# Kernel optimization log

Measured on AMD Instinct MI355X. Metric: run time of the kernel, lower is better.

## Reference

```python
import jax, jax.numpy as jnp
import numpy as np

N_Q = 9      # qubits -> state dim 512
N_L = 10     # circuit layers
DIM = 2 ** N_Q
B = 16384    # batch
N_CLS = 10


def _apply_1q(psi, U, q):
    # psi: [B, 2,...,2] (N_Q qubit axes); U: [2,2] complex
    psi = jnp.moveaxis(psi, q + 1, 1)
    shp = psi.shape
    psi = jnp.einsum('ij,bjk->bik', U, psi.reshape(shp[0], 2, -1)).reshape(shp)
    return jnp.moveaxis(psi, 1, q + 1)


def _apply_2q(psi, U, q0, q1):
    # U: [4,4] complex acting on (q0, q1)
    psi = jnp.moveaxis(psi, (q0 + 1, q1 + 1), (1, 2))
    shp = psi.shape
    psi = jnp.einsum('ij,bjk->bik', U, psi.reshape(shp[0], 4, -1)).reshape(shp)
    return jnp.moveaxis(psi, (1, 2), (q0 + 1, q1 + 1))


def _rot_mat(phi, theta, omega):
    # PennyLane Rot = RZ(omega) RY(theta) RZ(phi)
    c, s = jnp.cos(theta / 2), jnp.sin(theta / 2)
    a, b = (phi + omega) / 2, (phi - omega) / 2
    return jnp.stack([
        jnp.stack([jnp.exp(-1j * a) * c, -jnp.exp(1j * b) * s]),
        jnp.stack([jnp.exp(-1j * b) * s, jnp.exp(1j * a) * c]),
    ]).astype(jnp.complex64)


def _crx_mat(t):
    c, s = jnp.cos(t / 2), jnp.sin(t / 2)
    rx = jnp.stack([jnp.stack([c + 0j, -1j * s]),
                    jnp.stack([-1j * s, c + 0j])]).astype(jnp.complex64)
    return jnp.eye(4, dtype=jnp.complex64).at[2:, 2:].set(rx)


def _layer(psi, rot_n, crx_n):
    for i in range(N_Q):
        psi = _apply_1q(psi, _rot_mat(rot_n[i, 0], rot_n[i, 1], rot_n[i, 2]), i)
    for i in range(N_Q):
        psi = _apply_2q(psi, _crx_mat(crx_n[i, 0]), i, (i + 1) % N_Q)
    return psi


def _circuit(x, rot, crx):
    # AmplitudeEmbedding(normalize=True)
    psi = (x / jnp.linalg.norm(x, axis=1, keepdims=True)).astype(jnp.complex64)
    psi = psi.reshape((x.shape[0],) + (2,) * N_Q)
    for n in range(N_L):
        psi = _layer(psi, rot[n], crx[n])
    probs = psi.real ** 2 + psi.imag ** 2
    # <Z_q> = P(bit_q = 0) - P(bit_q = 1)
    zs = []
    for q in range(N_Q):
        axes = tuple(a for a in range(1, N_Q + 1) if a != q + 1)
        p = probs.sum(axis=axes)  # [B, 2]
        zs.append(p[:, 0] - p[:, 1])
    return jnp.stack(zs, axis=1)  # [B, N_Q]


def setup_inputs() -> dict:
    key = jax.random.key(0)
    k0, k1, k2, k3, k4 = jax.random.split(key, 5)
    x = jax.random.normal(k0, (B, DIM), jnp.float32)
    rot = jax.random.normal(k1, (N_L, N_Q, 3), jnp.float32)
    crx = jax.random.normal(k2, (N_L, N_Q, 1), jnp.float32)
    fc_w = jax.random.normal(k3, (N_CLS, N_Q), jnp.float32) * 0.3
    fc_b = jax.random.normal(k4, (N_CLS,), jnp.float32) * 0.1
    return {"x": x, "rot": rot, "crx": crx, "fc_w": fc_w, "fc_b": fc_b}


def reference(x, rot, crx, fc_w, fc_b):
    z = _circuit(x, rot, crx)          # [B, 9]
    logits = z @ fc_w.T + fc_b         # [B, 10]
    return jax.nn.log_softmax(logits, axis=1)
```

## Files before the change

### kernel.cpp

```cpp
#include <hip/hip_runtime.h>
#include <hip/hip_bf16.h>
#include <math.h>

#define NQ 9
#define NL 10
#define DIM 512
#define NCLS 10
#define B_TOT 16384

#define A_OFF   ((size_t)0)
#define BT_OFF  ((size_t)16 << 20)
#define ZP_OFF  ((size_t)32 << 20)
#define WS_NEED (((size_t)96) << 20)

__device__ __forceinline__ float shx(float v, int m) { return __shfl_xor(v, m, 64); }

__device__ __forceinline__ int looks_bf16(const void* p, int count) {
  const unsigned short* u = (const unsigned short*)p;
  int n = count < 64 ? count : 64;
  int good = 0;
  for (int i = 0; i < n; ++i) {
    unsigned short v = u[i];
    int e = (v >> 7) & 0xFF;
    good += (e >= 100 && e <= 140) || ((v & 0x7FFF) == 0);
  }
  return good * 8 >= n * 7;
}

__device__ __forceinline__ float ld(const void* p, int i, int isbf) {
  if (isbf) return __uint_as_float(((unsigned)((const unsigned short*)p)[i]) << 16);
  return ((const float*)p)[i];
}

template<int M>
__device__ __forceinline__ void rot_x(float (&sr)[8], float (&si)[8], const float* u) {
  float4 uA = *(const float4*)u;
  float4 uB = *(const float4*)(u + 4);
  bool hi = (threadIdx.x & M) != 0;
  float ar = hi ? uB.z : uA.x, ai = hi ? uB.w : uA.y;
  float br = hi ? uB.x : uA.z, bi = hi ? uB.y : uA.w;
#pragma unroll
  for (int r = 0; r < 8; ++r) {
    float pr = shx(sr[r], M), pi = shx(si[r], M);
    float nr = ar * sr[r] - ai * si[r] + br * pr - bi * pi;
    float ni = ar * si[r] + ai * sr[r] + br * pi + bi * pr;
    sr[r] = nr; si[r] = ni;
  }
}
template<int S>
__device__ __forceinline__ void rot_r(float (&sr)[8], float (&si)[8], const float* u) {
  float4 uA = *(const float4*)u;
  float4 uB = *(const float4*)(u + 4);
#pragma unroll
  for (int r0 = 0; r0 < 8; ++r0) {
    if (r0 & S) continue;
    int r1 = r0 + S;
    float a0r = sr[r0], a0i = si[r0], a1r = sr[r1], a1i = si[r1];
    sr[r0] = uA.x * a0r - uA.y * a0i + uA.z * a1r - uA.w * a1i;
    si[r0] = uA.x * a0i + uA.y * a0r + uA.z * a1i + uA.w * a1r;
    sr[r1] = uB.x * a0r - uB.y * a0i + uB.z * a1r - uB.w * a1i;
    si[r1] = uB.x * a0i + uB.y * a0r + uB.z * a1i + uB.w * a1r;
  }
}
template<int MC, int MT>
__device__ __forceinline__ void crx_ll(float (&sr)[8], float (&si)[8], const float* cs) {
  bool ctrl = (threadIdx.x & MC) != 0;
  float c = ctrl ? cs[0] : 1.0f;
  float s = ctrl ? cs[1] : 0.0f;
#pragma unroll
  for (int r = 0; r < 8; ++r) {
    float pr = shx(sr[r], MT), pi = shx(si[r], MT);
    float nr = c * sr[r] + s * pi;
    float ni = c * si[r] - s * pr;
    sr[r] = nr; si[r] = ni;
  }
}
template<int MC, int ST>
__device__ __forceinline__ void crx_lr(float (&sr)[8], float (&si)[8], const float* cs) {
  bool ctrl = (threadIdx.x & MC) != 0;
  float c = ctrl ? cs[0] : 1.0f;
  float s = ctrl ? cs[1] : 0.0f;
#pragma unroll
  for (int r0 = 0; r0 < 8; ++r0) {
    if (r0 & ST) continue;
    int r1 = r0 + ST;
    float a0r = sr[r0], a0i = si[r0], a1r = sr[r1], a1i = si[r1];
    sr[r0] = c * a0r + s * a1i;  si[r0] = c * a0i - s * a1r;
    sr[r1] = c * a1r + s * a0i;  si[r1] = c * a1i - s * a0r;
  }
}
template<int PC, int ST>
__device__ __forceinline__ void crx_rr(float (&sr)[8], float (&si)[8], const float* cs) {
  float c = cs[0], s = cs[1];
#pragma unroll
  for (int r0 = 0; r0 < 8; ++r0) {
    if (r0 & ST) continue;
    if (!((r0 >> PC) & 1)) continue;
    int r1 = r0 + ST;
    float a0r = sr[r0], a0i = si[r0], a1r = sr[r1], a1i = si[r1];
    sr[r0] = c * a0r + s * a1i;  si[r0] = c * a0i - s * a1r;
    sr[r1] = c * a1r + s * a0i;  si[r1] = c * a1i - s * a0r;
  }
}
template<int PC, int MT>
__device__ __forceinline__ void crx_rl(float (&sr)[8], float (&si)[8], const float* cs) {
  float c = cs[0], s = cs[1];
#pragma unroll
  for (int r = 0; r < 8; ++r) {
    if (!((r >> PC) & 1)) continue;
    float pr = shx(sr[r], MT), pi = shx(si[r], MT);
    float nr = c * sr[r] + s * pi;
    float ni = c * si[r] - s * pr;
    sr[r] = nr; si[r] = ni;
  }
}

__device__ __forceinline__ void build_gates(const void* rot, const void* crx,
                                            float* gU, float* gCS) {
  int tid = threadIdx.x;
  __shared__ int gflags[2];
  if (tid == 0) {
    gflags[0] = looks_bf16(rot, NL * NQ * 3);
    gflags[1] = looks_bf16(crx, NL * NQ);
  }
  __syncthreads();
  if (tid < NL * NQ) {
    int frot = gflags[0], fcrx = gflags[1];
    float phi = ld(rot, tid * 3 + 0, frot);
    float th  = ld(rot, tid * 3 + 1, frot);
    float om  = ld(rot, tid * 3 + 2, frot);
    float c = cosf(0.5f * th), s = sinf(0.5f * th);
    float a = 0.5f * (phi + om), b = 0.5f * (phi - om);
    float ca = cosf(a), sa = sinf(a), cb = cosf(b), sb = sinf(b);
    float* u = gU + tid * 8;
    u[0] =  ca * c; u[1] = -sa * c;
    u[2] = -cb * s; u[3] = -sb * s;
    u[4] =  cb * s; u[5] = -sb * s;
    u[6] =  ca * c; u[7] =  sa * c;
    float t2 = 0.5f * ld(crx, tid, fcrx);
    gCS[tid * 2 + 0] = cosf(t2);
    gCS[tid * 2 + 1] = sinf(t2);
  }
  __syncthreads();
}

__device__ __forceinline__ void run_circuit(float (&sr)[8], float (&si)[8],
                                            const float* gU, const float* gCS) {
#pragma unroll 1
  for (int n = 0; n < NL; ++n) {
    const float* U  = gU  + n * NQ * 8;
    const float* CS = gCS + n * NQ * 2;
    rot_x<32>(sr, si, U + 0 * 8);
    rot_x<16>(sr, si, U + 1 * 8);
    rot_x< 8>(sr, si, U + 2 * 8);
    rot_x< 4>(sr, si, U + 3 * 8);
    rot_x< 2>(sr, si, U + 4 * 8);
    rot_x< 1>(sr, si, U + 5 * 8);
    rot_r< 4>(sr, si, U + 6 * 8);
    rot_r< 2>(sr, si, U + 7 * 8);
    rot_r< 1>(sr, si, U + 8 * 8);
    crx_ll<32, 16>(sr, si, CS + 0 * 2);
    crx_ll<16,  8>(sr, si, CS + 1 * 2);
    crx_ll< 8,  4>(sr, si, CS + 2 * 2);
    crx_ll< 4,  2>(sr, si, CS + 3 * 2);
    crx_ll< 2,  1>(sr, si, CS + 4 * 2);
    crx_lr< 1,  4>(sr, si, CS + 5 * 2);
    crx_rr< 2,  2>(sr, si, CS + 6 * 2);
    crx_rr< 1,  1>(sr, si, CS + 7 * 2);
    crx_rl< 0, 32>(sr, si, CS + 8 * 2);
  }
}

template<int M>
__device__ __forceinline__ void rot_lane2(float (&sr)[2], float (&si)[2], const float* u) {
  float4 uA = *(const float4*)u;
  float4 uB = *(const float4*)(u + 4);
  bool hi = (threadIdx.x & M) != 0;
  float ar = hi ? uB.z : uA.x, ai = hi ? uB.w : uA.y;
  float br = hi ? uB.x : uA.z, bi = hi ? uB.y : uA.w;
#pragma unroll
  for (int r = 0; r < 2; ++r) {
    float pr = shx(sr[r], M), pi = shx(si[r], M);
    float nr = ar * sr[r] - ai * si[r] + br * pr - bi * pi;
    float ni = ar * si[r] + ai * sr[r] + br * pi + bi * pr;
    sr[r] = nr; si[r] = ni;
  }
}
__device__ __forceinline__ void rot_reg2(float (&sr)[2], float (&si)[2], const float* u) {
  float4 uA = *(const float4*)u;
  float4 uB = *(const float4*)(u + 4);
  float a0r = sr[0], a0i = si[0], a1r = sr[1], a1i = si[1];
  sr[0] = uA.x * a0r - uA.y * a0i + uA.z * a1r - uA.w * a1i;
  si[0] = uA.x * a0i + uA.y * a0r + uA.z * a1i + uA.w * a1r;
  sr[1] = uB.x * a0r - uB.y * a0i + uB.z * a1r - uB.w * a1i;
  si[1] = uB.x * a0i + uB.y * a0r + uB.z * a1i + uB.w * a1r;
}
__device__ __forceinline__ void crx_lane2(float (&sr)[2], float (&si)[2],
                                          float c, float s, int MT) {
#pragma unroll
  for (int r = 0; r < 2; ++r) {
    float pr = shx(sr[r], MT), pi = shx(si[r], MT);
    float nr = c * sr[r] + s * pi;
    float ni = c * si[r] - s * pr;
    sr[r] = nr; si[r] = ni;
  }
}
__device__ __forceinline__ void crx_reg2(float (&sr)[2], float (&si)[2], float c, float s) {
  float a0r = sr[0], a0i = si[0], a1r = sr[1], a1i = si[1];
  sr[0] = c * a0r + s * a1i;  si[0] = c * a0i - s * a1r;
  sr[1] = c * a1r + s * a0i;  si[1] = c * a1i - s * a0r;
}

__global__ __launch_bounds__(256) void prep_kernel(const void* __restrict__ x,
                                                   const void* __restrict__ rot,
                                                   const void* __restrict__ crx,
                                                   __hip_bfloat16* __restrict__ A,
                                                   __hip_bfloat16* __restrict__ BT) {
  int tid = threadIdx.x;
  if (blockIdx.x < DIM) {
    __shared__ __align__(16) float gU[NL * NQ * 8];
    __shared__ __align__(16) float gCS[NL * NQ * 2];
    __shared__ float sRe[DIM], sIm[DIM];
    build_gates(rot, crx, gU, gCS);
    int lane = tid & 63, wv = tid >> 6;
    int idx0 = wv * 128 + lane * 2;
    int k = blockIdx.x;
    float sr[2], si[2];
    sr[0] = (idx0 == k) ? 1.f : 0.f;
    sr[1] = (idx0 + 1 == k) ? 1.f : 0.f;
    si[0] = si[1] = 0.f;
#pragma unroll 1
    for (int n = 0; n < NL; ++n) {
      const float* U  = gU  + n * NQ * 8;
      const float* CS = gCS + n * NQ * 2;
      __syncthreads();
      sRe[idx0] = sr[0]; sIm[idx0] = si[0];
      sRe[idx0 + 1] = sr[1]; sIm[idx0 + 1] = si[1];
      __syncthreads();
      {
        const float* U0 = U; const float* U1 = U + 8;
        int a = wv >> 1, b = wv & 1;
        float mr[4], mi[4];
#pragma unroll
        for (int w2 = 0; w2 < 4; ++w2) {
          int a2 = w2 >> 1, b2 = w2 & 1;
          float u0r = U0[(a * 2 + a2) * 2], u0i = U0[(a * 2 + a2) * 2 + 1];
          float u1r = U1[(b * 2 + b2) * 2], u1i = U1[(b * 2 + b2) * 2 + 1];
          mr[w2] = u0r * u1r - u0i * u1i;
          mi[w2] = u0r * u1i + u0i * u1r;
        }
#pragma unroll
        for (int r = 0; r < 2; ++r) {
          float nr = 0.f, ni = 0.f;
#pragma unroll
          for (int w2 = 0; w2 < 4; ++w2) {
            float xr = sRe[w2 * 128 + lane * 2 + r];
            float xi = sIm[w2 * 128 + lane * 2 + r];
            nr += mr[w2] * xr - mi[w2] * xi;
            ni += mr[w2] * xi + mi[w2] * xr;
          }
          sr[r] = nr; si[r] = ni;
        }
      }
      rot_lane2<32>(sr, si, U + 2 * 8);
      rot_lane2<16>(sr, si, U + 3 * 8);
      rot_lane2< 8>(sr, si, U + 4 * 8);
      rot_lane2< 4>(sr, si, U + 5 * 8);
      rot_lane2< 2>(sr, si, U + 6 * 8);
      rot_lane2< 1>(sr, si, U + 7 * 8);
      rot_reg2(sr, si, U + 8 * 8);
      __syncthreads();
      sRe[idx0] = sr[0]; sIm[idx0] = si[0];
      sRe[idx0 + 1] = sr[1]; sIm[idx0 + 1] = si[1];
      __syncthreads();
      {
        float c = (wv & 2) ? CS[0] : 1.f, s = (wv & 2) ? CS[1] : 0.f;
        int p0 = (wv ^ 1) * 128 + lane * 2;
#pragma unroll
        for (int r = 0; r < 2; ++r) {
          float pr = sRe[p0 + r], pi = sIm[p0 + r];
          float nr = c * sr[r] + s * pi;
          float ni = c * si[r] - s * pr;
          sr[r] = nr; si[r] = ni;
        }
      }
      { float c = (wv & 1) ? CS[2] : 1.f, s = (wv & 1) ? CS[3] : 0.f;
        crx_lane2(sr, si, c, s, 32); }
      { bool ct = (lane & 32); crx_lane2(sr, si, ct ? CS[4] : 1.f, ct ? CS[5] : 0.f, 16); }
      { bool ct = (lane & 16); crx_lane2(sr, si, ct ? CS[6] : 1.f, ct ? CS[7] : 0.f, 8); }
      { bool ct = (lane &  8); crx_lane2(sr, si, ct ? CS[8] : 1.f, ct ? CS[9] : 0.f, 4); }
      { bool ct = (lane &  4); crx_lane2(sr, si, ct ? CS[10] : 1.f, ct ? CS[11] : 0.f, 2); }
      { bool ct = (lane &  2); crx_lane2(sr, si, ct ? CS[12] : 1.f, ct ? CS[13] : 0.f, 1); }
      { bool ct = (lane & 1); crx_reg2(sr, si, ct ? CS[14] : 1.f, ct ? CS[15] : 0.f); }
      __syncthreads();
      sRe[idx0] = sr[0]; sIm[idx0] = si[0];
      sRe[idx0 + 1] = sr[1]; sIm[idx0 + 1] = si[1];
      __syncthreads();
      {
        float c = CS[16], s = CS[17];
        int p1 = (wv ^ 2) * 128 + lane * 2 + 1;
        float pr = sRe[p1], pi = sIm[p1];
        float nr = c * sr[1] + s * pi;
        float ni = c * si[1] - s * pr;
        sr[1] = nr; si[1] = ni;
      }
    }
#pragma unroll
    for (int r = 0; r < 2; ++r) {
      int j = idx0 + r;
      BT[(size_t)j * DIM + k]         = __float2bfloat16(sr[r]);
      BT[(size_t)(DIM + j) * DIM + k] = __float2bfloat16(si[r]);
    }
  } else {
    __shared__ int fx;
    if (tid == 0) fx = looks_bf16(x, B_TOT * DIM);
    __syncthreads();
    size_t i0 = ((size_t)(blockIdx.x - DIM) * 256 + tid) * 8;
    if (fx) {
      *(uint4*)(A + i0) = *(const uint4*)((const unsigned short*)x + i0);
    } else {
      const float4* src = (const float4*)((const float*)x + i0);
      float4 a = src[0], b = src[1];
      __hip_bfloat16 o[8];
      o[0] = __float2bfloat16(a.x); o[1] = __float2bfloat16(a.y);
      o[2] = __float2bfloat16(a.z); o[3] = __float2bfloat16(a.w);
      o[4] = __float2bfloat16(b.x); o[5] = __float2bfloat16(b.y);
      o[6] = __float2bfloat16(b.z); o[7] = __float2bfloat16(b.w);
      *(uint4*)(A + i0) = *(uint4*)o;
    }
  }
}

using frag8 = __attribute__((ext_vector_type(8))) short;
using frag4 = __attribute__((ext_vector_type(4))) float;

typedef __attribute__((address_space(1))) const unsigned int GU32;
typedef __attribute__((address_space(3))) unsigned int LU32;
__device__ __forceinline__ void async16(const void* g, void* l) {
  __builtin_amdgcn_global_load_lds((GU32*)g, (LU32*)l, 16, 0, 0);
}

#define PPITCH 136
#define PANEL (128 * 32)

__global__ __launch_bounds__(256) void gemm_z_kernel(const unsigned short* __restrict__ A,
                                                     const unsigned short* __restrict__ BT,
                                                     float* __restrict__ Zp) {
  __shared__ __align__(16) unsigned short lsm[128 * PPITCH + 16 * PPITCH];
  unsigned short* lA0 = lsm;
  unsigned short* lA1 = lsm + PANEL;
  unsigned short* lB0 = lsm + 2 * PANEL;
  unsigned short* lB1 = lsm + 3 * PANEL;
  unsigned short* pA  = lsm;
  unsigned short* STm = lsm + 128 * PPITCH;
  int bid = blockIdx.x;
  int xcd = bid & 7;
  int slot = bid >> 3;
  int n0 = (slot & 7) * 128;
  int m0 = (xcd * 16 + (slot >> 3)) * 128;
  int tid = threadIdx.x;
  int wv = tid >> 6, lane = tid & 63;
  int wm = wv >> 1, wn = wv & 1;
  int row = lane & 15, quad = lane >> 4;
  for (int i = tid; i < 16 * 128; i += 256) {
    int q = i >> 7, k2 = i & 127;
    int j = (n0 + k2) & 511;
    float sg = (q < 9) ? (((j >> (8 - q)) & 1) ? -1.f : 1.f) : (q == 9 ? 1.f : 0.f);
    __hip_bfloat16 h = __float2bfloat16(sg);
    STm[q * PPITCH + k2] = *(unsigned short*)&h;
  }
  int srow = wv * 32 + (lane >> 2);
  int scol = (lane & 3) * 8;
  const unsigned short* gA = A + (size_t)(m0 + srow) * 512 + scol;
  const unsigned short* gB = BT + (size_t)(n0 + srow) * 512 + scol;
  frag4 acc[4][4] = {};
#pragma unroll 1
  for (int k0 = 0; k0 < 512; k0 += 64) {
    __syncthreads();
    async16(gA + k0,                 &lA0[(wv * 32) * 32]);
    async16(gA + k0 + 16 * 512,      &lA0[(wv * 32 + 16) * 32]);
    async16(gA + k0 + 32,            &lA1[(wv * 32) * 32]);
    async16(gA + k0 + 32 + 16 * 512, &lA1[(wv * 32 + 16) * 32]);
    async16(gB + k0,                 &lB0[(wv * 32) * 32]);
    async16(gB + k0 + 16 * 512,      &lB0[(wv * 32 + 16) * 32]);
    async16(gB + k0 + 32,            &lB1[(wv * 32) * 32]);
    async16(gB + k0 + 32 + 16 * 512, &lB1[(wv * 32 + 16) * 32]);
    __syncthreads();
    {
      frag8 af[4], bf[4];
#pragma unroll
      for (int i = 0; i < 4; ++i) {
        af[i] = *(const frag8*)(&lA0[(wm * 64 + i * 16 + row) * 32 + quad * 8]);
        bf[i] = *(const frag8*)(&lB0[(wn * 64 + i * 16 + row) * 32 + quad * 8]);
      }
#pragma unroll
      for (int mi = 0; mi < 4; ++mi)
#pragma unroll
        for (int ni = 0; ni < 4; ++ni)
          acc[mi][ni] = __builtin_amdgcn_mfma_f32_16x16x32_bf16(af[mi], bf[ni],
                                                                acc[mi][ni], 0, 0, 0);
    }
    {
      frag8 af[4], bf[4];
#pragma unroll
      for (int i = 0; i < 4; ++i) {
        af[i] = *(const frag8*)(&lA1[(wm * 64 + i * 16 + row) * 32 + quad * 8]);
        bf[i] = *(const frag8*)(&lB1[(wn * 64 + i * 16 + row) * 32 + quad * 8]);
      }
#pragma unroll
      for (int mi = 0; mi < 4; ++mi)
#pragma unroll
        for (int ni = 0; ni < 4; ++ni)
          acc[mi][ni] = __builtin_amdgcn_mfma_f32_16x16x32_bf16(af[mi], bf[ni],
                                                                acc[mi][ni], 0, 0, 0);
    }
  }
  __syncthreads();
#pragma unroll
  for (int mi = 0; mi < 4; ++mi)
#pragma unroll
    for (int ni = 0; ni < 4; ++ni)
#pragma unroll
      for (int rg = 0; rg < 4; ++rg) {
        float v = acc[mi][ni][rg];
        float p = v * v;
        int mrow = wm * 64 + mi * 16 + quad * 4 + rg;
        int k2 = wn * 64 + ni * 16 + row;
        __hip_bfloat16 h = __float2bfloat16(p);
        pA[mrow * PPITCH + k2] = *(unsigned short*)&h;
      }
  __syncthreads();
  frag8 b2[4];
#pragma unroll
  for (int kk = 0; kk < 4; ++kk)
    b2[kk] = *(const frag8*)(&STm[row * PPITCH + kk * 32 + quad * 8]);
  frag4 zacc2[2] = {};
#pragma unroll
  for (int t = 0; t < 2; ++t) {
    int mt = wv + t * 4;
#pragma unroll
    for (int kk = 0; kk < 4; ++kk) {
      frag8 a2 = *(const frag8*)(&pA[(mt * 16 + row) * PPITCH + kk * 32 + quad * 8]);
      zacc2[t] = __builtin_amdgcn_mfma_f32_16x16x32_bf16(a2, b2[kk], zacc2[t], 0, 0, 0);
    }
  }
  int panel = n0 >> 7;
  if (row < 10) {
#pragma unroll
    for (int t = 0; t < 2; ++t) {
      int mt = wv + t * 4;
#pragma unroll
      for (int rg = 0; rg < 4; ++rg) {
        int mrow = m0 + mt * 16 + quad * 4 + rg;
        Zp[(size_t)panel * (B_TOT * 10) + (size_t)mrow * 10 + row] = zacc2[t][rg];
      }
    }
  }
}

__global__ __launch_bounds__(256) void zred_kernel(const float* __restrict__ Zp,
                                                   const void* __restrict__ fcw,
                                                   const void* __restrict__ fcb,
                                                   float* __restrict__ out) {
  __shared__ int flags[2];
  __shared__ float sW[NCLS * NQ];
  __shared__ float sB[NCLS];
  int tid = threadIdx.x;
  if (tid == 0) {
    flags[0] = looks_bf16(fcw, NCLS * NQ);
    flags[1] = looks_bf16(fcb, NCLS);
  }
  __syncthreads();
  if (tid < NCLS * NQ) sW[tid] = ld(fcw, tid, flags[0]);
  if (tid < NCLS)      sB[tid] = ld(fcb, tid, flags[1]);
  __syncthreads();
  int row = blockIdx.x * 256 + tid;
  float z[10];
#pragma unroll
  for (int q = 0; q < 10; ++q) z[q] = 0.f;
#pragma unroll
  for (int pnl = 0; pnl < 8; ++pnl) {
    const float* p = Zp + (size_t)pnl * (B_TOT * 10) + (size_t)row * 10;
#pragma unroll
    for (int q = 0; q < 10; ++q) z[q] += p[q];
  }
  float invP = 1.0f / z[9];
#pragma unroll
  for (int q = 0; q < NQ; ++q) z[q] *= invP;
  float lg[NCLS], mx = -1e30f;
#pragma unroll
  for (int k = 0; k < NCLS; ++k) {
    float t = sB[k];
#pragma unroll
    for (int q = 0; q < NQ; ++q) t += z[q] * sW[k * NQ + q];
    lg[k] = t; mx = fmaxf(mx, t);
  }
  float se = 0.f;
#pragma unroll
  for (int k = 0; k < NCLS; ++k) se += expf(lg[k] - mx);
  float lse = mx + logf(se);
#pragma unroll
  for (int k = 0; k < NCLS; ++k) out[(size_t)row * NCLS + k] = lg[k] - lse;
}

__global__ __launch_bounds__(256) void qnn_kernel(
    const void* __restrict__ x, const void* __restrict__ rot,
    const void* __restrict__ crx, const void* __restrict__ fcw,
    const void* __restrict__ fcb, float* __restrict__ out) {
  __shared__ __align__(16) float gU[NL * NQ * 8];
  __shared__ __align__(16) float gCS[NL * NQ * 2];
  __shared__ int flags[3];
  int tid = threadIdx.x;
  if (tid == 0) {
    flags[0] = looks_bf16(x, B_TOT * DIM);
    flags[1] = looks_bf16(fcw, NCLS * NQ);
    flags[2] = looks_bf16(fcb, NCLS);
  }
  build_gates(rot, crx, gU, gCS);
  __syncthreads();
  int wid = (blockIdx.x * blockDim.x + tid) >> 6;
  int lane = tid & 63;
  float sr[8], si[8];
  if (flags[0]) {
    const uint4 u = *(const uint4*)((const unsigned short*)x + (size_t)wid * DIM + lane * 8);
    sr[0] = __uint_as_float(u.x << 16); sr[1] = __uint_as_float(u.x & 0xffff0000u);
    sr[2] = __uint_as_float(u.y << 16); sr[3] = __uint_as_float(u.y & 0xffff0000u);
    sr[4] = __uint_as_float(u.z << 16); sr[5] = __uint_as_float(u.z & 0xffff0000u);
    sr[6] = __uint_as_float(u.w << 16); sr[7] = __uint_as_float(u.w & 0xffff0000u);
  } else {
    const float4* xf = (const float4*)((const float*)x + (size_t)wid * DIM) + lane * 2;
    float4 a = xf[0], b = xf[1];
    sr[0] = a.x; sr[1] = a.y; sr[2] = a.z; sr[3] = a.w;
    sr[4] = b.x; sr[5] = b.y; sr[6] = b.z; sr[7] = b.w;
  }
  float nrm = 0.f;
#pragma unroll
  for (int r = 0; r < 8; ++r) { nrm += sr[r] * sr[r]; si[r] = 0.f; }
#pragma unroll
  for (int m = 1; m < 64; m <<= 1) nrm += shx(nrm, m);
  float inv = rsqrtf(nrm);
  inv = inv * (1.5f - 0.5f * nrm * inv * inv);
#pragma unroll
  for (int r = 0; r < 8; ++r) sr[r] *= inv;
  run_circuit(sr, si, gU, gCS);
  float p[8], P = 0.f;
#pragma unroll
  for (int r = 0; r < 8; ++r) { p[r] = sr[r] * sr[r] + si[r] * si[r]; P += p[r]; }
  float z[NQ];
#pragma unroll
  for (int q = 0; q < 6; ++q) z[q] = (lane & (32 >> q)) ? -P : P;
  z[6] = z[7] = z[8] = 0.f;
#pragma unroll
  for (int r = 0; r < 8; ++r) {
    z[6] += (r & 4) ? -p[r] : p[r];
    z[7] += (r & 2) ? -p[r] : p[r];
    z[8] += (r & 1) ? -p[r] : p[r];
  }
#pragma unroll
  for (int m = 1; m < 64; m <<= 1) {
#pragma unroll
    for (int q = 0; q < NQ; ++q) z[q] += shx(z[q], m);
  }
  int ffw = flags[1], ffb = flags[2];
  float lg[NCLS], mx = -1e30f;
#pragma unroll
  for (int k = 0; k < NCLS; ++k) {
    float t = ld(fcb, k, ffb);
#pragma unroll
    for (int q = 0; q < NQ; ++q) t += z[q] * ld(fcw, k * NQ + q, ffw);
    lg[k] = t; mx = fmaxf(mx, t);
  }
  float se = 0.f;
#pragma unroll
  for (int k = 0; k < NCLS; ++k) se += expf(lg[k] - mx);
  float lse = mx + logf(se);
  if (lane < NCLS) out[(size_t)wid * NCLS + lane] = lg[lane] - lse;
}

extern "C" void kernel_launch(void* const* d_in, const int* in_sizes, int n_in,
                              void* d_out, int out_size, void* d_ws, size_t ws_size,
                              hipStream_t stream) {
  const void* x   = d_in[0];
  const void* rot = d_in[1];
  const void* crx = d_in[2];
  const void* fcw = d_in[3];
  const void* fcb = d_in[4];
  float* out = (float*)d_out;
  if (ws_size >= WS_NEED) {
    __hip_bfloat16* A  = (__hip_bfloat16*)((char*)d_ws + A_OFF);
    __hip_bfloat16* BT = (__hip_bfloat16*)((char*)d_ws + BT_OFF);
    float*          Zp = (float*)((char*)d_ws + ZP_OFF);
    prep_kernel<<<DIM + (B_TOT * DIM) / (256 * 8), 256, 0, stream>>>(x, rot, crx, A, BT);
    gemm_z_kernel<<<(B_TOT / 128) * (1024 / 128), 256, 0, stream>>>(
        (const unsigned short*)A, (const unsigned short*)BT, Zp);
    zred_kernel<<<B_TOT / 256, 256, 0, stream>>>(Zp, fcw, fcb, out);
  } else {
    qnn_kernel<<<(B_TOT * 64) / 256, 256, 0, stream>>>(x, rot, crx, fcw, fcb, out);
  }
}
```

Before: 142.0 us.

## Use 512-thread blocks with fused 3-qubit gate matrices in unitary prep

The prep kernel now uses 512 threads, one amplitude per thread, instead of 256 threads holding two each. It precomputes 8x8 fused matrices for the first three Rot gates and for the first two CRX gates, and folds the last CRX of each layer into the next layer's load. This cuts the number of shared-memory round trips and barriers per layer. In exchange each thread does more multiply-adds per fused stage, the block uses more shared memory, and the conversion blocks are halved in count but doubled in size.

```diff
diff --git a/kernel.cpp b/kernel.cpp
--- a/kernel.cpp
+++ b/kernel.cpp
@@ -172,46 +172,25 @@
 }
 
 template<int M>
-__device__ __forceinline__ void rot_lane2(float (&sr)[2], float (&si)[2], const float* u) {
+__device__ __forceinline__ void rot1(float& sr, float& si, const float* u) {
   float4 uA = *(const float4*)u;
   float4 uB = *(const float4*)(u + 4);
   bool hi = (threadIdx.x & M) != 0;
   float ar = hi ? uB.z : uA.x, ai = hi ? uB.w : uA.y;
   float br = hi ? uB.x : uA.z, bi = hi ? uB.y : uA.w;
-#pragma unroll
-  for (int r = 0; r < 2; ++r) {
-    float pr = shx(sr[r], M), pi = shx(si[r], M);
-    float nr = ar * sr[r] - ai * si[r] + br * pr - bi * pi;
-    float ni = ar * si[r] + ai * sr[r] + br * pi + bi * pr;
-    sr[r] = nr; si[r] = ni;
-  }
-}
-__device__ __forceinline__ void rot_reg2(float (&sr)[2], float (&si)[2], const float* u) {
-  float4 uA = *(const float4*)u;
-  float4 uB = *(const float4*)(u + 4);
-  float a0r = sr[0], a0i = si[0], a1r = sr[1], a1i = si[1];
-  sr[0] = uA.x * a0r - uA.y * a0i + uA.z * a1r - uA.w * a1i;
-  si[0] = uA.x * a0i + uA.y * a0r + uA.z * a1i + uA.w * a1r;
-  sr[1] = uB.x * a0r - uB.y * a0i + uB.z * a1r - uB.w * a1i;
-  si[1] = uB.x * a0i + uB.y * a0r + uB.z * a1i + uB.w * a1r;
-}
-__device__ __forceinline__ void crx_lane2(float (&sr)[2], float (&si)[2],
-                                          float c, float s, int MT) {
-#pragma unroll
-  for (int r = 0; r < 2; ++r) {
-    float pr = shx(sr[r], MT), pi = shx(si[r], MT);
-    float nr = c * sr[r] + s * pi;
-    float ni = c * si[r] - s * pr;
-    sr[r] = nr; si[r] = ni;
-  }
-}
-__device__ __forceinline__ void crx_reg2(float (&sr)[2], float (&si)[2], float c, float s) {
-  float a0r = sr[0], a0i = si[0], a1r = sr[1], a1i = si[1];
-  sr[0] = c * a0r + s * a1i;  si[0] = c * a0i - s * a1r;
-  sr[1] = c * a1r + s * a0i;  si[1] = c * a1i - s * a0r;
-}
-
-__global__ __launch_bounds__(256) void prep_kernel(const void* __restrict__ x,
+  float pr = shx(sr, M), pi = shx(si, M);
+  float nr = ar * sr - ai * si + br * pr - bi * pi;
+  float ni = ar * si + ai * sr + br * pi + bi * pr;
+  sr = nr; si = ni;
+}
+__device__ __forceinline__ void crx1(float& sr, float& si, float c, float s, int MT) {
+  float pr = shx(sr, MT), pi = shx(si, MT);
+  float nr = c * sr + s * pi;
+  float ni = c * si - s * pr;
+  sr = nr; si = ni;
+}
+
+__global__ __launch_bounds__(512) void prep_kernel(const void* __restrict__ x,
                                                    const void* __restrict__ rot,
                                                    const void* __restrict__ crx,
                                                    __hip_bfloat16* __restrict__ A,
@@ -220,102 +199,118 @@
   if (blockIdx.x < DIM) {
     __shared__ __align__(16) float gU[NL * NQ * 8];
     __shared__ __align__(16) float gCS[NL * NQ * 2];
-    __shared__ float sRe[DIM], sIm[DIM];
+    __shared__ __align__(16) float gM8[NL * 64 * 2];
+    __shared__ __align__(16) float gM8c[NL * 64 * 2];
+    __shared__ float bRe[2][DIM], bIm[2][DIM];
     build_gates(rot, crx, gU, gCS);
+    for (int it = tid; it < NL * 64; it += 512) {
+      int n = it >> 6, e = it & 63;
+      int w = e >> 3, w2 = e & 7;
+      int a = (w >> 2) & 1, b = (w >> 1) & 1, c = w & 1;
+      int a2 = (w2 >> 2) & 1, b2 = (w2 >> 1) & 1, c2 = w2 & 1;
+      const float* U0 = gU + (n * 9 + 0) * 8;
+      const float* U1 = gU + (n * 9 + 1) * 8;
+      const float* U2 = gU + (n * 9 + 2) * 8;
+      float r0 = U0[(a * 2 + a2) * 2],  i0 = U0[(a * 2 + a2) * 2 + 1];
+      float r1 = U1[(b * 2 + b2) * 2],  i1 = U1[(b * 2 + b2) * 2 + 1];
+      float r2 = U2[(c * 2 + c2) * 2],  i2 = U2[(c * 2 + c2) * 2 + 1];
+      float rr = r0 * r1 - i0 * i1, ri = r0 * i1 + i0 * r1;
+      gM8[(n * 64 + e) * 2]     = rr * r2 - ri * i2;
+      gM8[(n * 64 + e) * 2 + 1] = rr * i2 + ri * r2;
+      const float* CSn = gCS + n * 18;
+      float c1 = CSn[0], s1 = CSn[1], c2v = CSn[2], s2v = CSn[3];
+      float f1r, f1i, f2r, f2i;
+      if (a == 0) { f1r = (b == b2) ? 1.f : 0.f; f1i = 0.f; }
+      else        { f1r = (b == b2) ? c1 : 0.f;  f1i = (b == b2) ? 0.f : -s1; }
+      if (b == 0) { f2r = (c == c2) ? 1.f : 0.f; f2i = 0.f; }
+      else        { f2r = (c == c2) ? c2v : 0.f; f2i = (c == c2) ? 0.f : -s2v; }
+      float Mr = (a == a2) ? (f1r * f2r - f1i * f2i) : 0.f;
+      float Mi = (a == a2) ? (f1r * f2i + f1i * f2r) : 0.f;
+      gM8c[(n * 64 + e) * 2]     = Mr;
+      gM8c[(n * 64 + e) * 2 + 1] = Mi;
+    }
+    __syncthreads();
     int lane = tid & 63, wv = tid >> 6;
-    int idx0 = wv * 128 + lane * 2;
     int k = blockIdx.x;
-    float sr[2], si[2];
-    sr[0] = (idx0 == k) ? 1.f : 0.f;
-    sr[1] = (idx0 + 1 == k) ? 1.f : 0.f;
-    si[0] = si[1] = 0.f;
+    float sr = (tid == k) ? 1.f : 0.f, si = 0.f;
 #pragma unroll 1
     for (int n = 0; n < NL; ++n) {
-      const float* U  = gU  + n * NQ * 8;
-      const float* CS = gCS + n * NQ * 2;
+      const float* CS  = gCS + n * 18;
+      const float* CSp = gCS + (n - 1) * 18;
+      bRe[0][tid] = sr; bIm[0][tid] = si;
       __syncthreads();
-      sRe[idx0] = sr[0]; sIm[idx0] = si[0];
-      sRe[idx0 + 1] = sr[1]; sIm[idx0 + 1] = si[1];
+      float xr[8], xi[8];
+#pragma unroll
+      for (int w2 = 0; w2 < 8; ++w2) {
+        xr[w2] = bRe[0][w2 * 64 + lane];
+        xi[w2] = bIm[0][w2 * 64 + lane];
+      }
+      if (n > 0 && (lane & 1)) {
+        float cp = CSp[16], sp = CSp[17];
+        float tr[8], ti[8];
+#pragma unroll
+        for (int w2 = 0; w2 < 8; ++w2) {
+          tr[w2] = cp * xr[w2] + sp * xi[w2 ^ 4];
+          ti[w2] = cp * xi[w2] - sp * xr[w2 ^ 4];
+        }
+#pragma unroll
+        for (int w2 = 0; w2 < 8; ++w2) { xr[w2] = tr[w2]; xi[w2] = ti[w2]; }
+      }
+      {
+        const float* M = gM8 + n * 128 + wv * 16;
+        float nr = 0.f, ni = 0.f;
+#pragma unroll
+        for (int w2 = 0; w2 < 8; ++w2) {
+          float mr = M[w2 * 2], mi2 = M[w2 * 2 + 1];
+          nr += mr * xr[w2] - mi2 * xi[w2];
+          ni += mr * xi[w2] + mi2 * xr[w2];
+        }
+        sr = nr; si = ni;
+      }
+      rot1<32>(sr, si, gU + (n * 9 + 3) * 8);
+      rot1<16>(sr, si, gU + (n * 9 + 4) * 8);
+      rot1< 8>(sr, si, gU + (n * 9 + 5) * 8);
+      rot1< 4>(sr, si, gU + (n * 9 + 6) * 8);
+      rot1< 2>(sr, si, gU + (n * 9 + 7) * 8);
+      rot1< 1>(sr, si, gU + (n * 9 + 8) * 8);
+      bRe[1][tid] = sr; bIm[1][tid] = si;
       __syncthreads();
       {
-        const float* U0 = U; const float* U1 = U + 8;
-        int a = wv >> 1, b = wv & 1;
-        float mr[4], mi[4];
-#pragma unroll
-        for (int w2 = 0; w2 < 4; ++w2) {
-          int a2 = w2 >> 1, b2 = w2 & 1;
-          float u0r = U0[(a * 2 + a2) * 2], u0i = U0[(a * 2 + a2) * 2 + 1];
-          float u1r = U1[(b * 2 + b2) * 2], u1i = U1[(b * 2 + b2) * 2 + 1];
-          mr[w2] = u0r * u1r - u0i * u1i;
-          mi[w2] = u0r * u1i + u0i * u1r;
+        const float* M = gM8c + n * 128 + wv * 16;
+        float nr = 0.f, ni = 0.f;
+#pragma unroll
+        for (int w2 = 0; w2 < 8; ++w2) {
+          float vr = bRe[1][w2 * 64 + lane], vi = bIm[1][w2 * 64 + lane];
+          float mr = M[w2 * 2], mi2 = M[w2 * 2 + 1];
+          nr += mr * vr - mi2 * vi;
+          ni += mr * vi + mi2 * vr;
         }
-#pragma unroll
-        for (int r = 0; r < 2; ++r) {
-          float nr = 0.f, ni = 0.f;
-#pragma unroll
-          for (int w2 = 0; w2 < 4; ++w2) {
-            float xr = sRe[w2 * 128 + lane * 2 + r];
-            float xi = sIm[w2 * 128 + lane * 2 + r];
-            nr += mr[w2] * xr - mi[w2] * xi;
-            ni += mr[w2] * xi + mi[w2] * xr;
-          }
-          sr[r] = nr; si[r] = ni;
-        }
-      }
-      rot_lane2<32>(sr, si, U + 2 * 8);
-      rot_lane2<16>(sr, si, U + 3 * 8);
-      rot_lane2< 8>(sr, si, U + 4 * 8);
-      rot_lane2< 4>(sr, si, U + 5 * 8);
-      rot_lane2< 2>(sr, si, U + 6 * 8);
-      rot_lane2< 1>(sr, si, U + 7 * 8);
-      rot_reg2(sr, si, U + 8 * 8);
-      __syncthreads();
-      sRe[idx0] = sr[0]; sIm[idx0] = si[0];
-      sRe[idx0 + 1] = sr[1]; sIm[idx0 + 1] = si[1];
-      __syncthreads();
-      {
-        float c = (wv & 2) ? CS[0] : 1.f, s = (wv & 2) ? CS[1] : 0.f;
-        int p0 = (wv ^ 1) * 128 + lane * 2;
-#pragma unroll
-        for (int r = 0; r < 2; ++r) {
-          float pr = sRe[p0 + r], pi = sIm[p0 + r];
-          float nr = c * sr[r] + s * pi;
-          float ni = c * si[r] - s * pr;
-          sr[r] = nr; si[r] = ni;
-        }
-      }
-      { float c = (wv & 1) ? CS[2] : 1.f, s = (wv & 1) ? CS[3] : 0.f;
-        crx_lane2(sr, si, c, s, 32); }
-      { bool ct = (lane & 32); crx_lane2(sr, si, ct ? CS[4] : 1.f, ct ? CS[5] : 0.f, 16); }
-      { bool ct = (lane & 16); crx_lane2(sr, si, ct ? CS[6] : 1.f, ct ? CS[7] : 0.f, 8); }
-      { bool ct = (lane &  8); crx_lane2(sr, si, ct ? CS[8] : 1.f, ct ? CS[9] : 0.f, 4); }
-      { bool ct = (lane &  4); crx_lane2(sr, si, ct ? CS[10] : 1.f, ct ? CS[11] : 0.f, 2); }
-      { bool ct = (lane &  2); crx_lane2(sr, si, ct ? CS[12] : 1.f, ct ? CS[13] : 0.f, 1); }
-      { bool ct = (lane & 1); crx_reg2(sr, si, ct ? CS[14] : 1.f, ct ? CS[15] : 0.f); }
-      __syncthreads();
-      sRe[idx0] = sr[0]; sIm[idx0] = si[0];
-      sRe[idx0 + 1] = sr[1]; sIm[idx0 + 1] = si[1];
-      __syncthreads();
-      {
-        float c = CS[16], s = CS[17];
-        int p1 = (wv ^ 2) * 128 + lane * 2 + 1;
-        float pr = sRe[p1], pi = sIm[p1];
-        float nr = c * sr[1] + s * pi;
-        float ni = c * si[1] - s * pr;
-        sr[1] = nr; si[1] = ni;
-      }
-    }
-#pragma unroll
-    for (int r = 0; r < 2; ++r) {
-      int j = idx0 + r;
-      BT[(size_t)j * DIM + k]         = __float2bfloat16(sr[r]);
-      BT[(size_t)(DIM + j) * DIM + k] = __float2bfloat16(si[r]);
-    }
+        sr = nr; si = ni;
+      }
+      { bool ct = wv & 1;    crx1(sr, si, ct ? CS[4] : 1.f,  ct ? CS[5] : 0.f, 32); }
+      { bool ct = lane & 32; crx1(sr, si, ct ? CS[6] : 1.f,  ct ? CS[7] : 0.f, 16); }
+      { bool ct = lane & 16; crx1(sr, si, ct ? CS[8] : 1.f,  ct ? CS[9] : 0.f,  8); }
+      { bool ct = lane &  8; crx1(sr, si, ct ? CS[10] : 1.f, ct ? CS[11] : 0.f, 4); }
+      { bool ct = lane &  4; crx1(sr, si, ct ? CS[12] : 1.f, ct ? CS[13] : 0.f, 2); }
+      { bool ct = lane &  2; crx1(sr, si, ct ? CS[14] : 1.f, ct ? CS[15] : 0.f, 1); }
+    }
+    bRe[0][tid] = sr; bIm[0][tid] = si;
+    __syncthreads();
+    if (lane & 1) {
+      const float* CS9 = gCS + (NL - 1) * 18;
+      float cp = CS9[16], sp = CS9[17];
+      float pr = bRe[0][(wv ^ 4) * 64 + lane], pi = bIm[0][(wv ^ 4) * 64 + lane];
+      float nr = cp * sr + sp * pi;
+      float ni = cp * si - sp * pr;
+      sr = nr; si = ni;
+    }
+    BT[(size_t)tid * DIM + k]         = __float2bfloat16(sr);
+    BT[(size_t)(DIM + tid) * DIM + k] = __float2bfloat16(si);
   } else {
     __shared__ int fx;
     if (tid == 0) fx = looks_bf16(x, B_TOT * DIM);
     __syncthreads();
-    size_t i0 = ((size_t)(blockIdx.x - DIM) * 256 + tid) * 8;
+    size_t i0 = ((size_t)(blockIdx.x - DIM) * 512 + tid) * 8;
     if (fx) {
       *(uint4*)(A + i0) = *(const uint4*)((const unsigned short*)x + i0);
     } else {
@@ -590,7 +585,7 @@
     __hip_bfloat16* A  = (__hip_bfloat16*)((char*)d_ws + A_OFF);
     __hip_bfloat16* BT = (__hip_bfloat16*)((char*)d_ws + BT_OFF);
     float*          Zp = (float*)((char*)d_ws + ZP_OFF);
-    prep_kernel<<<DIM + (B_TOT * DIM) / (256 * 8), 256, 0, stream>>>(x, rot, crx, A, BT);
+    prep_kernel<<<DIM + (B_TOT * DIM) / (512 * 8), 512, 0, stream>>>(x, rot, crx, A, BT);
     gemm_z_kernel<<<(B_TOT / 128) * (1024 / 128), 256, 0, stream>>>(
         (const unsigned short*)A, (const unsigned short*)BT, Zp);
     zred_kernel<<<B_TOT / 256, 256, 0, stream>>>(Zp, fcw, fcb, out);
```

New measurement: 147.9 us. 4.2% more time.
